# Optimization experiments

Measured on AMD Instinct MI355X. Metric: run time of the kernel, lower is better.

Reference implementation:

```python
import jax, jax.numpy as jnp
import numpy as np

B, N, F, H, N_ITERS = 64, 256, 16, 256, 10


def setup_inputs() -> dict:
    key = jax.random.key(0)
    ks = jax.random.split(key, 20)
    s = 0.05
    jets = jax.random.normal(ks[0], (B, N, F), dtype=jnp.float32)
    # row-normalized dense adjacency (D^-1 A style)
    a = jax.random.uniform(ks[1], (B, N, N), dtype=jnp.float32)
    dads = a / jnp.sum(a, axis=-1, keepdims=True)
    p = lambda k, sh: jax.random.normal(k, sh, dtype=jnp.float32) * s
    return {
        'jets': jets, 'dads': dads,
        'W_emb': p(ks[2], (F, H)), 'b_emb': jnp.zeros((H,), jnp.float32),
        'W_msg': p(ks[3], (H, H)), 'b_msg': jnp.zeros((H,), jnp.float32),
        # GRU vertex update: input = concat(message[H], s[F]) -> H
        'Wz': p(ks[4], (H + F, H)), 'Uz': p(ks[5], (H, H)), 'bz': jnp.zeros((H,), jnp.float32),
        'Wr': p(ks[6], (H + F, H)), 'Ur': p(ks[7], (H, H)), 'br': jnp.zeros((H,), jnp.float32),
        'Wh': p(ks[8], (H + F, H)), 'Uh': p(ks[9], (H, H)), 'bh': jnp.zeros((H,), jnp.float32),
        'W_r1': p(ks[10], (H, H)), 'b_r1': jnp.zeros((H,), jnp.float32),
        'W_r2': p(ks[11], (H, H)), 'b_r2': jnp.zeros((H,), jnp.float32),
    }


def reference(jets, dads, W_emb, b_emb, W_msg, b_msg,
              Wz, Uz, bz, Wr, Ur, br, Wh, Uh, bh,
              W_r1, b_r1, W_r2, b_r2):
    # Embedding: [B,N,F] -> [B,N,H]
    h = jnp.tanh(jets @ W_emb + b_emb)
    for _ in range(N_ITERS):
        # Message: linear then adjacency aggregation + tanh
        m = jnp.tanh(jnp.matmul(dads, h @ W_msg + b_msg))  # [B,N,H]
        # GRU-style vertex update; input = concat(message, original features s)
        x = jnp.concatenate([m, jets], axis=-1)            # [B,N,H+F]
        z = jax.nn.sigmoid(x @ Wz + h @ Uz + bz)
        r = jax.nn.sigmoid(x @ Wr + h @ Ur + br)
        h_tilde = jnp.tanh(x @ Wh + (r * h) @ Uh + bh)
        h = (1.0 - z) * h + z * h_tilde
    # Readout: per-node MLP then sum over nodes -> [B,H]
    out = jnp.sum(jnp.tanh(h @ W_r1 + b_r1) @ W_r2 + b_r2, axis=1)
    return out
```

## Files before the change

### kernel.cpp

```cpp
#include <hip/hip_runtime.h>

#define DEVI __device__ __forceinline__

typedef __attribute__((ext_vector_type(4))) float f32x4;
typedef __attribute__((ext_vector_type(8))) short s16x8;
typedef __attribute__((ext_vector_type(4))) short s16x4;
typedef unsigned short u16;
typedef unsigned int u32;

#define WST 288
#define SROW 264
#define AST 260

#define WAITVM(n) __builtin_amdgcn_s_waitcnt(((n)&0xF) | 0x70 | 0xF00 | (((n)>>4)<<14))

DEVI u16 f2bf(float x){
  u32 u = __float_as_uint(x);
  u = (u + 0x7fffu + ((u >> 16) & 1u)) >> 16;
  return (u16)u;
}
DEVI float bf2f(u16 v){ return __uint_as_float(((u32)v) << 16); }

DEVI float fsigm(float x){ return __builtin_amdgcn_rcpf(1.f + __builtin_amdgcn_exp2f(-1.442695041f * x)); }
DEVI float ftanh(float x){ float e = __builtin_amdgcn_exp2f(2.885390082f * x); return 1.f - 2.f * __builtin_amdgcn_rcpf(e + 1.f); }

DEVI s16x8 ld8(const u16* p){ return *(const s16x8*)p; }
DEVI s16x8 ldb64p(const u16* p){
  s16x4 lo = *(const s16x4*)p;
  s16x4 hi = *(const s16x4*)(p + 4);
  s16x8 r;
  r[0]=lo[0]; r[1]=lo[1]; r[2]=lo[2]; r[3]=lo[3];
  r[4]=hi[0]; r[5]=hi[1]; r[6]=hi[2]; r[7]=hi[3];
  return r;
}

DEVI f32x4 ld4bf(const u16* p){
  uint2 v = *(const uint2*)p;
  f32x4 r;
  r[0] = bf2f((u16)(v.x & 0xffff)); r[1] = bf2f((u16)(v.x >> 16));
  r[2] = bf2f((u16)(v.y & 0xffff)); r[3] = bf2f((u16)(v.y >> 16));
  return r;
}

DEVI void st4bf(u16* p, float a, float b, float c, float d){
  uint2 v;
  v.x = (u32)f2bf(a) | ((u32)f2bf(b) << 16);
  v.y = (u32)f2bf(c) | ((u32)f2bf(d) << 16);
  *(uint2*)p = v;
}

#define MFMA(a,b,c) __builtin_amdgcn_mfma_f32_16x16x32_bf16((a),(b),(c),0,0,0)

DEVI void dma_tile32(const u16* gbase, int rowStride, int c, u16* ldsbase, int lane){
#pragma unroll
  for(int q = 0; q < 2; q++){
    int rw  = lane >> 2;
    int col = ((lane & 3) ^ ((rw >> 1) & 3)) * 8;
    const u16* g = gbase + (size_t)(q*16 + rw)*rowStride + c*32 + col;
    __builtin_amdgcn_global_load_lds((__attribute__((address_space(1))) void*)g,
                                     (__attribute__((address_space(3))) void*)(ldsbase + q*512),
                                     16, 0, 0);
  }
}
#define AFRAG(buf, t) ld8(&(buf)[(t)*512 + ln*32 + ((qd ^ ((ln>>1)&3))*8)])

__global__ void k_prep(
  const float* __restrict__ jets, const float* __restrict__ dads, const float* __restrict__ W_emb,
  const float* __restrict__ W_msg, const float* __restrict__ Wz, const float* __restrict__ Uz,
  const float* __restrict__ Wr, const float* __restrict__ Ur, const float* __restrict__ Wh,
  const float* __restrict__ Uh, const float* __restrict__ W_r1,
  u16* __restrict__ jp, u16* __restrict__ dadsb, u16* __restrict__ Wet, u16* __restrict__ Wmt,
  u16* __restrict__ Wzt, u16* __restrict__ Uzt, u16* __restrict__ Wrt, u16* __restrict__ Urt,
  u16* __restrict__ Wht, u16* __restrict__ Uht, u16* __restrict__ Wr1t)
{
  int blk = blockIdx.x, tid = threadIdx.x;
  if(blk < 1280){
    int mi = blk >> 8, k = blk & 255, j = tid;
    const float* src; u16* dst;
    switch(mi){
      case 0: src = W_msg; dst = Wmt;  break;
      case 1: src = Uz;    dst = Uzt;  break;
      case 2: src = Ur;    dst = Urt;  break;
      case 3: src = Uh;    dst = Uht;  break;
      default: src = W_r1; dst = Wr1t; break;
    }
    dst[j*256 + k] = f2bf(src[k*256 + j]);
  } else if(blk < 2144){
    int q = blk - 1280; int mi = q / 288; int k = q - mi*288; int j = tid;
    const float* src; u16* dst;
    switch(mi){ case 0: src = Wz; dst = Wzt; break; case 1: src = Wr; dst = Wrt; break; default: src = Wh; dst = Wht; break; }
    dst[j*WST + k] = (k < 272) ? f2bf(src[k*256 + j]) : (u16)0;
  } else if(blk < 2176){
    int idx = (blk - 2144)*256 + tid;
    int j = idx >> 5, k = idx & 31;
    Wet[idx] = (k < 16) ? f2bf(W_emb[k*256 + j]) : (u16)0;
  } else if(blk < 4224){
    int idx = (blk - 2176)*256 + tid;
    int n = idx >> 5, k = idx & 31;
    jp[idx] = (k < 16) ? f2bf(jets[n*16 + k]) : (u16)0;
  } else {
    int idx = (blk - 4224)*256 + tid;
    f32x4 v = *(const f32x4*)(dads + (size_t)idx*4);
    st4bf(dadsb + (size_t)idx*4, v[0], v[1], v[2], v[3]);
  }
}

__global__ __launch_bounds__(256,3) void k_embed(
  u16* __restrict__ h, u16* __restrict__ hmo,
  const u16* __restrict__ jp, const u16* __restrict__ Wet, const float* __restrict__ be,
  const u16* __restrict__ Wmt, const float* __restrict__ bm)
{
  __shared__ u16 hbuf[16*SROW];
  const int tid = threadIdx.x;
  const int wv = tid >> 6, lane = tid & 63, ln = lane & 15, qd = lane >> 4;
  const int n0 = blockIdx.x * 16;
  const int b  = n0 >> 8;
  const int nb = n0 & 255;
  const int nodeA = n0 + ln;

  s16x8 jfr = ld8(jp + (size_t)nodeA*32 + qd*8);
#pragma unroll
  for(int t = 0; t < 4; t++){
    int j0 = (wv*4 + t) * 16;
    f32x4 acc = {0.f,0.f,0.f,0.f};
    s16x8 a = ld8(Wet + (size_t)(j0 + ln)*32 + qd*8);
    acc = MFMA(a, jfr, acc);
    f32x4 bv = *(const f32x4*)(be + j0 + qd*4);
    f32x4 hv;
#pragma unroll
    for(int r = 0; r < 4; r++) hv[r] = ftanh(acc[r] + bv[r]);
    st4bf(h + (size_t)nodeA*256 + j0 + qd*4, hv[0], hv[1], hv[2], hv[3]);
    st4bf(&hbuf[ln*SROW + j0 + qd*4], hv[0], hv[1], hv[2], hv[3]);
  }
  __syncthreads();

  s16x8 af[8];
#pragma unroll
  for(int c = 0; c < 8; c++) af[c] = ld8(&hbuf[ln*SROW + c*32 + qd*8]);
#pragma unroll
  for(int tp = 0; tp < 2; tp++){
    int j0 = (wv*4 + tp*2) * 16, j1 = j0 + 16;
    f32x4 a0 = {0.f,0.f,0.f,0.f}, a1 = {0.f,0.f,0.f,0.f};
#pragma unroll
    for(int c = 0; c < 8; c++){
      a0 = MFMA(af[c], ld8(Wmt + (size_t)(j0 + ln)*256 + c*32 + qd*8), a0);
      a1 = MFMA(af[c], ld8(Wmt + (size_t)(j1 + ln)*256 + c*32 + qd*8), a1);
    }
    float b0 = bm[j0 + ln], b1 = bm[j1 + ln];
    st4bf(hmo + (size_t)(b*256 + j0 + ln)*256 + nb + qd*4, a0[0]+b0, a0[1]+b0, a0[2]+b0, a0[3]+b0);
    st4bf(hmo + (size_t)(b*256 + j1 + ln)*256 + nb + qd*4, a1[0]+b1, a1[1]+b1, a1[2]+b1, a1[3]+b1);
  }
}

__global__ __launch_bounds__(512,1) void k_gru(
  u16* __restrict__ h,
  const u16* __restrict__ hmi, u16* __restrict__ hmo,
  const u16* __restrict__ dadsb, const u16* __restrict__ jp,
  const u16* __restrict__ Wzt, const u16* __restrict__ Wrt, const u16* __restrict__ Wht,
  const u16* __restrict__ Uzt, const u16* __restrict__ Urt, const u16* __restrict__ Uht,
  const u16* __restrict__ Wmt,
  const float* __restrict__ bz, const float* __restrict__ br, const float* __restrict__ bhb,
  const float* __restrict__ bm)
{
  __shared__ u16 smM[64*AST];
  __shared__ u16 smB[64*AST];
  __shared__ __align__(16) u16 stg[8][2][2][1024];
  const int tid = threadIdx.x;
  const int wv = tid >> 6, lane = tid & 63, ln = lane & 15, qd = lane >> 4;
  const int blk   = blockIdx.x;
  const int batch = (blk & 7) * 8 + (blk >> 5);
  const int group = (blk >> 3) & 3;
  const int n0 = batch * 256 + group * 64;
  const int b  = batch;
  const int nb = group * 64;
  const int j0w = wv * 32;

  u16* s0 = &stg[wv][0][0][0];
  u16* s1 = &stg[wv][1][0][0];
  u16* u0 = &stg[wv][0][1][0];
  u16* u1 = &stg[wv][1][1][0];

  s16x8 jB[4];
#pragma unroll
  for(int i = 0; i < 4; i++) jB[i] = ld8(jp + (size_t)(n0 + i*16 + ln)*32 + qd*8);

  {
    const u16* gA = hmi + (size_t)(b*256 + j0w)*256;
    f32x4 acc[2][4];
#pragma unroll
    for(int t = 0; t < 2; t++)
#pragma unroll
      for(int i = 0; i < 4; i++) acc[t][i] = (f32x4){0.f,0.f,0.f,0.f};
    dma_tile32(gA, 256, 0, s0, lane);
    s16x8 Bf[4], Bn[4];
#pragma unroll
    for(int i = 0; i < 4; i++) Bf[i] = ld8(dadsb + (size_t)(n0 + i*16 + ln)*256 + qd*8);
#pragma unroll
    for(int c = 0; c < 8; c++){
      u16* cur = (c & 1) ? s1 : s0;
      if(c < 7){
        dma_tile32(gA, 256, c+1, (c & 1) ? s0 : s1, lane);
#pragma unroll
        for(int i = 0; i < 4; i++) Bn[i] = ld8(dadsb + (size_t)(n0 + i*16 + ln)*256 + (c+1)*32 + qd*8);
        WAITVM(6);
      } else {
        WAITVM(0);
      }
#pragma unroll
      for(int t = 0; t < 2; t++){
        s16x8 A = AFRAG(cur, t);
#pragma unroll
        for(int i = 0; i < 4; i++) acc[t][i] = MFMA(A, Bf[i], acc[t][i]);
      }
      if(c < 7){
#pragma unroll
        for(int i = 0; i < 4; i++) Bf[i] = Bn[i];
      }
    }
#pragma unroll
    for(int t = 0; t < 2; t++)
#pragma unroll
      for(int i = 0; i < 4; i++)
        st4bf(&smM[(i*16 + ln)*AST + j0w + t*16 + qd*4],
              ftanh(acc[t][i][0]), ftanh(acc[t][i][1]), ftanh(acc[t][i][2]), ftanh(acc[t][i][3]));
  }
  __syncthreads();

  {
    const u16* gW = Wrt + (size_t)j0w*WST;
    const u16* gU = Urt + (size_t)j0w*256;
    f32x4 acc[2][4];
#pragma unroll
    for(int t = 0; t < 2; t++)
#pragma unroll
      for(int i = 0; i < 4; i++) acc[t][i] = (f32x4){0.f,0.f,0.f,0.f};
    s16x8 Aj[2];
#pragma unroll
    for(int t = 0; t < 2; t++) Aj[t] = ld8(Wrt + (size_t)(j0w + t*16 + ln)*WST + 256 + qd*8);
    dma_tile32(gW, WST, 0, s0, lane);
    dma_tile32(gU, 256, 0, u0, lane);
    s16x8 Bh[4], Bn[4];
#pragma unroll
    for(int i = 0; i < 4; i++) Bh[i] = ld8(h + (size_t)(n0 + i*16 + ln)*256 + qd*8);
#pragma unroll
    for(int c = 0; c < 8; c++){
      u16* cw = (c & 1) ? s1 : s0;
      u16* cu = (c & 1) ? u1 : u0;
      if(c < 7){
        dma_tile32(gW, WST, c+1, (c & 1) ? s0 : s1, lane);
        dma_tile32(gU, 256, c+1, (c & 1) ? u0 : u1, lane);
#pragma unroll
        for(int i = 0; i < 4; i++) Bn[i] = ld8(h + (size_t)(n0 + i*16 + ln)*256 + (c+1)*32 + qd*8);
        WAITVM(8);
      } else {
        WAITVM(0);
      }
      s16x8 Bm[4];
#pragma unroll
      for(int i = 0; i < 4; i++) Bm[i] = ldb64p(&smM[(i*16 + ln)*AST + c*32 + qd*8]);
#pragma unroll
      for(int t = 0; t < 2; t++){
        s16x8 Aw = AFRAG(cw, t);
#pragma unroll
        for(int i = 0; i < 4; i++) acc[t][i] = MFMA(Aw, Bm[i], acc[t][i]);
      }
#pragma unroll
      for(int t = 0; t < 2; t++){
        s16x8 Au = AFRAG(cu, t);
#pragma unroll
        for(int i = 0; i < 4; i++) acc[t][i] = MFMA(Au, Bh[i], acc[t][i]);
      }
      if(c < 7){
#pragma unroll
        for(int i = 0; i < 4; i++) Bh[i] = Bn[i];
      }
    }
#pragma unroll
    for(int t = 0; t < 2; t++)
#pragma unroll
      for(int i = 0; i < 4; i++) acc[t][i] = MFMA(Aj[t], jB[i], acc[t][i]);
#pragma unroll
    for(int t = 0; t < 2; t++){
      f32x4 bv = *(const f32x4*)(br + j0w + t*16 + qd*4);
#pragma unroll
      for(int i = 0; i < 4; i++){
        f32x4 hv = ld4bf(h + (size_t)(n0 + i*16 + ln)*256 + j0w + t*16 + qd*4);
        st4bf(&smB[(i*16 + ln)*AST + j0w + t*16 + qd*4],
              fsigm(acc[t][i][0]+bv[0])*hv[0], fsigm(acc[t][i][1]+bv[1])*hv[1],
              fsigm(acc[t][i][2]+bv[2])*hv[2], fsigm(acc[t][i][3]+bv[3])*hv[3]);
      }
    }
  }
  __syncthreads();

  f32x4 zacc[2][4], gacc[2][4];
#pragma unroll
  for(int t = 0; t < 2; t++)
#pragma unroll
    for(int i = 0; i < 4; i++) zacc[t][i] = (f32x4){0.f,0.f,0.f,0.f};
  {
    const u16* gW = Wzt + (size_t)j0w*WST;
    const u16* gU = Uzt + (size_t)j0w*256;
    s16x8 Aj[2];
#pragma unroll
    for(int t = 0; t < 2; t++) Aj[t] = ld8(Wzt + (size_t)(j0w + t*16 + ln)*WST + 256 + qd*8);
    dma_tile32(gW, WST, 0, s0, lane);
    dma_tile32(gU, 256, 0, u0, lane);
    s16x8 Bh[4], Bn[4];
#pragma unroll
    for(int i = 0; i < 4; i++) Bh[i] = ld8(h + (size_t)(n0 + i*16 + ln)*256 + qd*8);
#pragma unroll
    for(int c = 0; c < 8; c++){
      u16* cw = (c & 1) ? s1 : s0;
      u16* cu = (c & 1) ? u1 : u0;
      if(c < 7){
        dma_tile32(gW, WST, c+1, (c & 1) ? s0 : s1, lane);
        dma_tile32(gU, 256, c+1, (c & 1) ? u0 : u1, lane);
#pragma unroll
        for(int i = 0; i < 4; i++) Bn[i] = ld8(h + (size_t)(n0 + i*16 + ln)*256 + (c+1)*32 + qd*8);
        WAITVM(8);
      } else {
        WAITVM(0);
      }
      s16x8 Bm[4];
#pragma unroll
      for(int i = 0; i < 4; i++) Bm[i] = ldb64p(&smM[(i*16 + ln)*AST + c*32 + qd*8]);
#pragma unroll
      for(int t = 0; t < 2; t++){
        s16x8 Aw = AFRAG(cw, t);
#pragma unroll
        for(int i = 0; i < 4; i++) zacc[t][i] = MFMA(Aw, Bm[i], zacc[t][i]);
      }
#pragma unroll
      for(int t = 0; t < 2; t++){
        s16x8 Au = AFRAG(cu, t);
#pragma unroll
        for(int i = 0; i < 4; i++) zacc[t][i] = MFMA(Au, Bh[i], zacc[t][i]);
      }
      if(c < 7){
#pragma unroll
        for(int i = 0; i < 4; i++) Bh[i] = Bn[i];
      }
    }
#pragma unroll
    for(int t = 0; t < 2; t++)
#pragma unroll
      for(int i = 0; i < 4; i++) zacc[t][i] = MFMA(Aj[t], jB[i], zacc[t][i]);
  }

#pragma unroll
  for(int t = 0; t < 2; t++)
#pragma unroll
    for(int i = 0; i < 4; i++) gacc[t][i] = (f32x4){0.f,0.f,0.f,0.f};
  {
    const u16* gW = Wht + (size_t)j0w*WST;
    const u16* gU = Uht + (size_t)j0w*256;
    s16x8 Aj[2];
#pragma unroll
    for(int t = 0; t < 2; t++) Aj[t] = ld8(Wht + (size_t)(j0w + t*16 + ln)*WST + 256 + qd*8);
    dma_tile32(gW, WST, 0, s0, lane);
    dma_tile32(gU, 256, 0, u0, lane);
#pragma unroll
    for(int c = 0; c < 8; c++){
      u16* cw = (c & 1) ? s1 : s0;
      u16* cu = (c & 1) ? u1 : u0;
      if(c < 7){
        dma_tile32(gW, WST, c+1, (c & 1) ? s0 : s1, lane);
        dma_tile32(gU, 256, c+1, (c & 1) ? u0 : u1, lane);
        WAITVM(4);
      } else {
        WAITVM(0);
      }
      s16x8 Bm[4], Brh[4];
#pragma unroll
      for(int i = 0; i < 4; i++){
        Bm[i]  = ldb64p(&smM[(i*16 + ln)*AST + c*32 + qd*8]);
        Brh[i] = ldb64p(&smB[(i*16 + ln)*AST + c*32 + qd*8]);
      }
#pragma unroll
      for(int t = 0; t < 2; t++){
        s16x8 Aw = AFRAG(cw, t);
#pragma unroll
        for(int i = 0; i < 4; i++) gacc[t][i] = MFMA(Aw, Bm[i], gacc[t][i]);
      }
#pragma unroll
      for(int t = 0; t < 2; t++){
        s16x8 Au = AFRAG(cu, t);
#pragma unroll
        for(int i = 0; i < 4; i++) gacc[t][i] = MFMA(Au, Brh[i], gacc[t][i]);
      }
    }
#pragma unroll
    for(int t = 0; t < 2; t++)
#pragma unroll
      for(int i = 0; i < 4; i++) gacc[t][i] = MFMA(Aj[t], jB[i], gacc[t][i]);
  }
  __syncthreads();

#pragma unroll
  for(int t = 0; t < 2; t++){
    f32x4 bzv = *(const f32x4*)(bz + j0w + t*16 + qd*4);
    f32x4 bhv = *(const f32x4*)(bhb + j0w + t*16 + qd*4);
#pragma unroll
    for(int i = 0; i < 4; i++){
      f32x4 hv = ld4bf(h + (size_t)(n0 + i*16 + ln)*256 + j0w + t*16 + qd*4);
      f32x4 hn;
#pragma unroll
      for(int r = 0; r < 4; r++){
        float z  = fsigm(zacc[t][i][r] + bzv[r]);
        float th = ftanh(gacc[t][i][r] + bhv[r]);
        hn[r] = hv[r] + z * (th - hv[r]);
      }
      st4bf(h + (size_t)(n0 + i*16 + ln)*256 + j0w + t*16 + qd*4, hn[0], hn[1], hn[2], hn[3]);
      st4bf(&smM[(i*16 + ln)*AST + j0w + t*16 + qd*4], hn[0], hn[1], hn[2], hn[3]);
    }
  }
  __syncthreads();

  {
    const u16* gA = Wmt + (size_t)j0w*256;
    f32x4 acc[2][4];
#pragma unroll
    for(int t = 0; t < 2; t++)
#pragma unroll
      for(int i = 0; i < 4; i++) acc[t][i] = (f32x4){0.f,0.f,0.f,0.f};
    dma_tile32(gA, 256, 0, s0, lane);
#pragma unroll
    for(int c = 0; c < 8; c++){
      u16* cur = (c & 1) ? s1 : s0;
      if(c < 7){
        dma_tile32(gA, 256, c+1, (c & 1) ? s0 : s1, lane);
        WAITVM(2);
      } else {
        WAITVM(0);
      }
      s16x8 Bf[4];
#pragma unroll
      for(int i = 0; i < 4; i++) Bf[i] = ldb64p(&smM[(i*16 + ln)*AST + c*32 + qd*8]);
#pragma unroll
      for(int t = 0; t < 2; t++){
        s16x8 A = AFRAG(cur, t);
#pragma unroll
        for(int i = 0; i < 4; i++) acc[t][i] = MFMA(A, Bf[i], acc[t][i]);
      }
    }
#pragma unroll
    for(int t = 0; t < 2; t++){
      f32x4 bmv = *(const f32x4*)(bm + j0w + t*16 + qd*4);
#pragma unroll
      for(int i = 0; i < 4; i++){
#pragma unroll
        for(int r = 0; r < 4; r++){
          hmo[(size_t)(b*256 + j0w + t*16 + qd*4 + r)*256 + nb + i*16 + ln] =
            f2bf(acc[t][i][r] + bmv[r]);
        }
      }
    }
  }
}

__global__ __launch_bounds__(256,3) void k_t(
  const u16* __restrict__ h, u16* __restrict__ t_out,
  const u16* __restrict__ Wr1t, const float* __restrict__ br1)
{
  const int tid = threadIdx.x;
  const int wv = tid >> 6, lane = tid & 63, ln = lane & 15, qd = lane >> 4;
  const int n0 = blockIdx.x * 16;
  const int nodeA = n0 + ln;

  s16x8 hfr[8];
#pragma unroll
  for(int c = 0; c < 8; c++) hfr[c] = ld8(h + (size_t)nodeA*256 + c*32 + qd*8);
#pragma unroll
  for(int tp = 0; tp < 2; tp++){
    int j0 = (wv*4 + tp*2) * 16, j1 = j0 + 16;
    f32x4 a0 = {0.f,0.f,0.f,0.f}, a1 = {0.f,0.f,0.f,0.f};
#pragma unroll
    for(int c = 0; c < 8; c++){
      a0 = MFMA(ld8(Wr1t + (size_t)(j0 + ln)*256 + c*32 + qd*8), hfr[c], a0);
      a1 = MFMA(ld8(Wr1t + (size_t)(j1 + ln)*256 + c*32 + qd*8), hfr[c], a1);
    }
    f32x4 b0 = *(const f32x4*)(br1 + j0 + qd*4);
    f32x4 b1 = *(const f32x4*)(br1 + j1 + qd*4);
    st4bf(t_out + (size_t)nodeA*256 + j0 + qd*4,
          ftanh(a0[0]+b0[0]), ftanh(a0[1]+b0[1]), ftanh(a0[2]+b0[2]), ftanh(a0[3]+b0[3]));
    st4bf(t_out + (size_t)nodeA*256 + j1 + qd*4,
          ftanh(a1[0]+b1[0]), ftanh(a1[1]+b1[1]), ftanh(a1[2]+b1[2]), ftanh(a1[3]+b1[3]));
  }
}

__global__ void k_sum(const u16* __restrict__ t, float* __restrict__ s4){
  int blk = blockIdx.x, tid = threadIdx.x;
  int b = blk >> 2, q = blk & 3;
  float acc = 0.f;
  for(int i = 0; i < 64; i++){
    int n = q*64 + i;
    acc += bf2f(t[(size_t)(b*256 + n)*256 + tid]);
  }
  s4[blk*256 + tid] = acc;
}

__global__ void k_out(const float* __restrict__ s4, const float* __restrict__ W_r2,
                      const float* __restrict__ b_r2, float* __restrict__ out){
  int b = blockIdx.x, j = threadIdx.x;
  float acc = 256.f * b_r2[j];
  for(int k = 0; k < 256; k++){
    float sv = s4[(b*4+0)*256 + k] + s4[(b*4+1)*256 + k] + s4[(b*4+2)*256 + k] + s4[(b*4+3)*256 + k];
    acc += sv * W_r2[k*256 + j];
  }
  out[b*256 + j] = acc;
}

extern "C" void kernel_launch(void* const* d_in, const int* in_sizes, int n_in,
                              void* d_out, int out_size, void* d_ws, size_t ws_size,
                              hipStream_t stream)
{
  const float* jets  = (const float*)d_in[0];
  const float* dads  = (const float*)d_in[1];
  const float* W_emb = (const float*)d_in[2];
  const float* b_emb = (const float*)d_in[3];
  const float* W_msg = (const float*)d_in[4];
  const float* b_msg = (const float*)d_in[5];
  const float* Wz    = (const float*)d_in[6];
  const float* Uz    = (const float*)d_in[7];
  const float* bz    = (const float*)d_in[8];
  const float* Wr    = (const float*)d_in[9];
  const float* Ur    = (const float*)d_in[10];
  const float* br    = (const float*)d_in[11];
  const float* Wh    = (const float*)d_in[12];
  const float* Uh    = (const float*)d_in[13];
  const float* bh    = (const float*)d_in[14];
  const float* W_r1  = (const float*)d_in[15];
  const float* b_r1  = (const float*)d_in[16];
  const float* W_r2  = (const float*)d_in[17];
  const float* b_r2  = (const float*)d_in[18];

  char* ws = (char*)d_ws;
  u16* h      = (u16*)(ws);
  u16* hmA    = (u16*)(ws + 8388608);
  u16* hmB    = (u16*)(ws + 16777216);
  u16* dadsb  = (u16*)(ws + 25165824);
  u16* jp     = (u16*)(ws + 33554432);
  u16* Wmt    = (u16*)(ws + 34603008);
  u16* Uzt    = (u16*)(ws + 34734080);
  u16* Urt    = (u16*)(ws + 34865152);
  u16* Uht    = (u16*)(ws + 34996224);
  u16* Wr1t   = (u16*)(ws + 35127296);
  u16* Wzt    = (u16*)(ws + 35258368);
  u16* Wrt    = (u16*)(ws + 35405824);
  u16* Wht    = (u16*)(ws + 35553280);
  u16* Wet    = (u16*)(ws + 35700736);
  float* s4   = (float*)(ws + 35717120);
  float* outp = (float*)d_out;

  k_prep<<<8320, 256, 0, stream>>>(jets, dads, W_emb, W_msg, Wz, Uz, Wr, Ur, Wh, Uh, W_r1,
                                   jp, dadsb, Wet, Wmt, Wzt, Uzt, Wrt, Urt, Wht, Uht, Wr1t);
  k_embed<<<1024, 256, 0, stream>>>(h, hmA, jp, Wet, b_emb, Wmt, b_msg);
  for(int it = 0; it < 10; ++it){
    const u16* hin = (it & 1) ? hmB : hmA;
    u16* hout      = (it & 1) ? hmA : hmB;
    k_gru<<<256, 512, 0, stream>>>(h, hin, hout, dadsb, jp,
                                   Wzt, Wrt, Wht, Uzt, Urt, Uht, Wmt,
                                   bz, br, bh, b_msg);
  }
  k_t<<<1024, 256, 0, stream>>>(h, hmB, Wr1t, b_r1);
  k_sum<<<256, 256, 0, stream>>>(hmB, s4);
  k_out<<<64, 256, 0, stream>>>(s4, W_r2, b_r2, outp);
}
```

Before: 605.7 us.

## Prefetch next-phase weight tiles before barriers, widen LDS loads, fuse readout kernels

Weight-tile DMA for each GRU phase now starts before the preceding __syncthreads, so the global-to-LDS transfer overlaps the barrier and the epilogue of the previous phase. Per-lane DMA addresses are computed once and reused across chunks. The LDS row stride becomes 264, which allows single 128-bit reads of the smM/smB fragments instead of two 64-bit halves, at some risk of bank conflicts. The k_sum and k_out readout kernels are merged into one launch with 64 blocks, trading parallelism in the node sum for one fewer launch.

```diff
diff --git a/kernel.cpp b/kernel.cpp
--- a/kernel.cpp
+++ b/kernel.cpp
@@ -4,13 +4,12 @@
 
 typedef __attribute__((ext_vector_type(4))) float f32x4;
 typedef __attribute__((ext_vector_type(8))) short s16x8;
-typedef __attribute__((ext_vector_type(4))) short s16x4;
 typedef unsigned short u16;
 typedef unsigned int u32;
 
 #define WST 288
 #define SROW 264
-#define AST 260
+#define AST 264
 
 #define WAITVM(n) __builtin_amdgcn_s_waitcnt(((n)&0xF) | 0x70 | 0xF00 | (((n)>>4)<<14))
 
@@ -25,14 +24,6 @@
 DEVI float ftanh(float x){ float e = __builtin_amdgcn_exp2f(2.885390082f * x); return 1.f - 2.f * __builtin_amdgcn_rcpf(e + 1.f); }
 
 DEVI s16x8 ld8(const u16* p){ return *(const s16x8*)p; }
-DEVI s16x8 ldb64p(const u16* p){
-  s16x4 lo = *(const s16x4*)p;
-  s16x4 hi = *(const s16x4*)(p + 4);
-  s16x8 r;
-  r[0]=lo[0]; r[1]=lo[1]; r[2]=lo[2]; r[3]=lo[3];
-  r[4]=hi[0]; r[5]=hi[1]; r[6]=hi[2]; r[7]=hi[3];
-  return r;
-}
 
 DEVI f32x4 ld4bf(const u16* p){
   uint2 v = *(const uint2*)p;
@@ -51,13 +42,11 @@
 
 #define MFMA(a,b,c) __builtin_amdgcn_mfma_f32_16x16x32_bf16((a),(b),(c),0,0,0)
 
-DEVI void dma_tile32(const u16* gbase, int rowStride, int c, u16* ldsbase, int lane){
+DEVI void dma2(const u16* lanebase, int rowStrideElems, int c, u16* ldsbase){
 #pragma unroll
   for(int q = 0; q < 2; q++){
-    int rw  = lane >> 2;
-    int col = ((lane & 3) ^ ((rw >> 1) & 3)) * 8;
-    const u16* g = gbase + (size_t)(q*16 + rw)*rowStride + c*32 + col;
-    __builtin_amdgcn_global_load_lds((__attribute__((address_space(1))) void*)g,
+    const u16* g = lanebase + (size_t)q*16*rowStrideElems + c*32;
+    __builtin_amdgcn_global_load_lds((__attribute__((address_space(1))) const void*)g,
                                      (__attribute__((address_space(3))) void*)(ldsbase + q*512),
                                      16, 0, 0);
   }
@@ -180,18 +169,22 @@
   u16* u0 = &stg[wv][0][1][0];
   u16* u1 = &stg[wv][1][1][0];
 
+  const int rw = lane >> 2;
+  const int cs = ((lane & 3) ^ ((lane >> 3) & 3)) * 8;
+
+  const u16* laneA = hmi + (size_t)(b*256 + j0w + rw)*256 + cs;
+  dma2(laneA, 256, 0, s0);
+
   s16x8 jB[4];
 #pragma unroll
   for(int i = 0; i < 4; i++) jB[i] = ld8(jp + (size_t)(n0 + i*16 + ln)*32 + qd*8);
 
   {
-    const u16* gA = hmi + (size_t)(b*256 + j0w)*256;
     f32x4 acc[2][4];
 #pragma unroll
     for(int t = 0; t < 2; t++)
 #pragma unroll
       for(int i = 0; i < 4; i++) acc[t][i] = (f32x4){0.f,0.f,0.f,0.f};
-    dma_tile32(gA, 256, 0, s0, lane);
     s16x8 Bf[4], Bn[4];
 #pragma unroll
     for(int i = 0; i < 4; i++) Bf[i] = ld8(dadsb + (size_t)(n0 + i*16 + ln)*256 + qd*8);
@@ -199,7 +192,7 @@
     for(int c = 0; c < 8; c++){
       u16* cur = (c & 1) ? s1 : s0;
       if(c < 7){
-        dma_tile32(gA, 256, c+1, (c & 1) ? s0 : s1, lane);
+        dma2(laneA, 256, c+1, (c & 1) ? s0 : s1);
 #pragma unroll
         for(int i = 0; i < 4; i++) Bn[i] = ld8(dadsb + (size_t)(n0 + i*16 + ln)*256 + (c+1)*32 + qd*8);
         WAITVM(6);
@@ -224,11 +217,13 @@
         st4bf(&smM[(i*16 + ln)*AST + j0w + t*16 + qd*4],
               ftanh(acc[t][i][0]), ftanh(acc[t][i][1]), ftanh(acc[t][i][2]), ftanh(acc[t][i][3]));
   }
+  const u16* laneWr = Wrt + (size_t)(j0w + rw)*WST + cs;
+  const u16* laneUr = Urt + (size_t)(j0w + rw)*256 + cs;
+  dma2(laneWr, WST, 0, s0);
+  dma2(laneUr, 256, 0, u0);
   __syncthreads();
 
   {
-    const u16* gW = Wrt + (size_t)j0w*WST;
-    const u16* gU = Urt + (size_t)j0w*256;
     f32x4 acc[2][4];
 #pragma unroll
     for(int t = 0; t < 2; t++)
@@ -237,8 +232,6 @@
     s16x8 Aj[2];
 #pragma unroll
     for(int t = 0; t < 2; t++) Aj[t] = ld8(Wrt + (size_t)(j0w + t*16 + ln)*WST + 256 + qd*8);
-    dma_tile32(gW, WST, 0, s0, lane);
-    dma_tile32(gU, 256, 0, u0, lane);
     s16x8 Bh[4], Bn[4];
 #pragma unroll
     for(int i = 0; i < 4; i++) Bh[i] = ld8(h + (size_t)(n0 + i*16 + ln)*256 + qd*8);
@@ -247,8 +240,8 @@
       u16* cw = (c & 1) ? s1 : s0;
       u16* cu = (c & 1) ? u1 : u0;
       if(c < 7){
-        dma_tile32(gW, WST, c+1, (c & 1) ? s0 : s1, lane);
-        dma_tile32(gU, 256, c+1, (c & 1) ? u0 : u1, lane);
+        dma2(laneWr, WST, c+1, (c & 1) ? s0 : s1);
+        dma2(laneUr, 256, c+1, (c & 1) ? u0 : u1);
 #pragma unroll
         for(int i = 0; i < 4; i++) Bn[i] = ld8(h + (size_t)(n0 + i*16 + ln)*256 + (c+1)*32 + qd*8);
         WAITVM(8);
@@ -257,7 +250,7 @@
       }
       s16x8 Bm[4];
 #pragma unroll
-      for(int i = 0; i < 4; i++) Bm[i] = ldb64p(&smM[(i*16 + ln)*AST + c*32 + qd*8]);
+      for(int i = 0; i < 4; i++) Bm[i] = ld8(&smM[(i*16 + ln)*AST + c*32 + qd*8]);
 #pragma unroll
       for(int t = 0; t < 2; t++){
         s16x8 Aw = AFRAG(cw, t);
@@ -291,6 +284,10 @@
       }
     }
   }
+  const u16* laneWz = Wzt + (size_t)(j0w + rw)*WST + cs;
+  const u16* laneUz = Uzt + (size_t)(j0w + rw)*256 + cs;
+  dma2(laneWz, WST, 0, s0);
+  dma2(laneUz, 256, 0, u0);
   __syncthreads();
 
   f32x4 zacc[2][4], gacc[2][4];
@@ -299,13 +296,9 @@
 #pragma unroll
     for(int i = 0; i < 4; i++) zacc[t][i] = (f32x4){0.f,0.f,0.f,0.f};
   {
-    const u16* gW = Wzt + (size_t)j0w*WST;
-    const u16* gU = Uzt + (size_t)j0w*256;
     s16x8 Aj[2];
 #pragma unroll
     for(int t = 0; t < 2; t++) Aj[t] = ld8(Wzt + (size_t)(j0w + t*16 + ln)*WST + 256 + qd*8);
-    dma_tile32(gW, WST, 0, s0, lane);
-    dma_tile32(gU, 256, 0, u0, lane);
     s16x8 Bh[4], Bn[4];
 #pragma unroll
     for(int i = 0; i < 4; i++) Bh[i] = ld8(h + (size_t)(n0 + i*16 + ln)*256 + qd*8);
@@ -314,8 +307,8 @@
       u16* cw = (c & 1) ? s1 : s0;
       u16* cu = (c & 1) ? u1 : u0;
       if(c < 7){
-        dma_tile32(gW, WST, c+1, (c & 1) ? s0 : s1, lane);
-        dma_tile32(gU, 256, c+1, (c & 1) ? u0 : u1, lane);
+        dma2(laneWz, WST, c+1, (c & 1) ? s0 : s1);
+        dma2(laneUz, 256, c+1, (c & 1) ? u0 : u1);
 #pragma unroll
         for(int i = 0; i < 4; i++) Bn[i] = ld8(h + (size_t)(n0 + i*16 + ln)*256 + (c+1)*32 + qd*8);
         WAITVM(8);
@@ -324,7 +317,7 @@
       }
       s16x8 Bm[4];
 #pragma unroll
-      for(int i = 0; i < 4; i++) Bm[i] = ldb64p(&smM[(i*16 + ln)*AST + c*32 + qd*8]);
+      for(int i = 0; i < 4; i++) Bm[i] = ld8(&smM[(i*16 + ln)*AST + c*32 + qd*8]);
 #pragma unroll
       for(int t = 0; t < 2; t++){
         s16x8 Aw = AFRAG(cw, t);
@@ -347,26 +340,27 @@
 #pragma unroll
       for(int i = 0; i < 4; i++) zacc[t][i] = MFMA(Aj[t], jB[i], zacc[t][i]);
   }
+
+  const u16* laneWh = Wht + (size_t)(j0w + rw)*WST + cs;
+  const u16* laneUh = Uht + (size_t)(j0w + rw)*256 + cs;
+  dma2(laneWh, WST, 0, s0);
+  dma2(laneUh, 256, 0, u0);
 
 #pragma unroll
   for(int t = 0; t < 2; t++)
 #pragma unroll
     for(int i = 0; i < 4; i++) gacc[t][i] = (f32x4){0.f,0.f,0.f,0.f};
   {
-    const u16* gW = Wht + (size_t)j0w*WST;
-    const u16* gU = Uht + (size_t)j0w*256;
     s16x8 Aj[2];
 #pragma unroll
     for(int t = 0; t < 2; t++) Aj[t] = ld8(Wht + (size_t)(j0w + t*16 + ln)*WST + 256 + qd*8);
-    dma_tile32(gW, WST, 0, s0, lane);
-    dma_tile32(gU, 256, 0, u0, lane);
 #pragma unroll
     for(int c = 0; c < 8; c++){
       u16* cw = (c & 1) ? s1 : s0;
       u16* cu = (c & 1) ? u1 : u0;
       if(c < 7){
-        dma_tile32(gW, WST, c+1, (c & 1) ? s0 : s1, lane);
-        dma_tile32(gU, 256, c+1, (c & 1) ? u0 : u1, lane);
+        dma2(laneWh, WST, c+1, (c & 1) ? s0 : s1);
+        dma2(laneUh, 256, c+1, (c & 1) ? u0 : u1);
         WAITVM(4);
       } else {
         WAITVM(0);
@@ -374,8 +368,8 @@
       s16x8 Bm[4], Brh[4];
 #pragma unroll
       for(int i = 0; i < 4; i++){
-        Bm[i]  = ldb64p(&smM[(i*16 + ln)*AST + c*32 + qd*8]);
-        Brh[i] = ldb64p(&smB[(i*16 + ln)*AST + c*32 + qd*8]);
+        Bm[i]  = ld8(&smM[(i*16 + ln)*AST + c*32 + qd*8]);
+        Brh[i] = ld8(&smB[(i*16 + ln)*AST + c*32 + qd*8]);
       }
 #pragma unroll
       for(int t = 0; t < 2; t++){
@@ -395,6 +389,8 @@
 #pragma unroll
       for(int i = 0; i < 4; i++) gacc[t][i] = MFMA(Aj[t], jB[i], gacc[t][i]);
   }
+  const u16* laneWm = Wmt + (size_t)(j0w + rw)*256 + cs;
+  dma2(laneWm, 256, 0, s0);
   __syncthreads();
 
 #pragma unroll
@@ -418,25 +414,23 @@
   __syncthreads();
 
   {
-    const u16* gA = Wmt + (size_t)j0w*256;
     f32x4 acc[2][4];
 #pragma unroll
     for(int t = 0; t < 2; t++)
 #pragma unroll
       for(int i = 0; i < 4; i++) acc[t][i] = (f32x4){0.f,0.f,0.f,0.f};
-    dma_tile32(gA, 256, 0, s0, lane);
 #pragma unroll
     for(int c = 0; c < 8; c++){
       u16* cur = (c & 1) ? s1 : s0;
       if(c < 7){
-        dma_tile32(gA, 256, c+1, (c & 1) ? s0 : s1, lane);
+        dma2(laneWm, 256, c+1, (c & 1) ? s0 : s1);
         WAITVM(2);
       } else {
         WAITVM(0);
       }
       s16x8 Bf[4];
 #pragma unroll
-      for(int i = 0; i < 4; i++) Bf[i] = ldb64p(&smM[(i*16 + ln)*AST + c*32 + qd*8]);
+      for(int i = 0; i < 4; i++) Bf[i] = ld8(&smM[(i*16 + ln)*AST + c*32 + qd*8]);
 #pragma unroll
       for(int t = 0; t < 2; t++){
         s16x8 A = AFRAG(cur, t);
@@ -489,26 +483,18 @@
   }
 }
 
-__global__ void k_sum(const u16* __restrict__ t, float* __restrict__ s4){
-  int blk = blockIdx.x, tid = threadIdx.x;
-  int b = blk >> 2, q = blk & 3;
+__global__ void k_red(const u16* __restrict__ t, const float* __restrict__ W_r2,
+                      const float* __restrict__ b_r2, float* __restrict__ out){
+  __shared__ float s[256];
+  int b = blockIdx.x, k = threadIdx.x;
   float acc = 0.f;
-  for(int i = 0; i < 64; i++){
-    int n = q*64 + i;
-    acc += bf2f(t[(size_t)(b*256 + n)*256 + tid]);
-  }
-  s4[blk*256 + tid] = acc;
-}
-
-__global__ void k_out(const float* __restrict__ s4, const float* __restrict__ W_r2,
-                      const float* __restrict__ b_r2, float* __restrict__ out){
-  int b = blockIdx.x, j = threadIdx.x;
-  float acc = 256.f * b_r2[j];
-  for(int k = 0; k < 256; k++){
-    float sv = s4[(b*4+0)*256 + k] + s4[(b*4+1)*256 + k] + s4[(b*4+2)*256 + k] + s4[(b*4+3)*256 + k];
-    acc += sv * W_r2[k*256 + j];
-  }
-  out[b*256 + j] = acc;
+  for(int n = 0; n < 256; n++) acc += bf2f(t[(size_t)(b*256 + n)*256 + k]);
+  s[k] = acc;
+  __syncthreads();
+  int j = threadIdx.x;
+  float o = 256.f * b_r2[j];
+  for(int k2 = 0; k2 < 256; k2++) o += s[k2] * W_r2[k2*256 + j];
+  out[b*256 + j] = o;
 }
 
 extern "C" void kernel_launch(void* const* d_in, const int* in_sizes, int n_in,
@@ -550,7 +536,6 @@
   u16* Wrt    = (u16*)(ws + 35405824);
   u16* Wht    = (u16*)(ws + 35553280);
   u16* Wet    = (u16*)(ws + 35700736);
-  float* s4   = (float*)(ws + 35717120);
   float* outp = (float*)d_out;
 
   k_prep<<<8320, 256, 0, stream>>>(jets, dads, W_emb, W_msg, Wz, Uz, Wr, Ur, Wh, Uh, W_r1,
@@ -564,6 +549,5 @@
                                    bz, br, bh, b_msg);
   }
   k_t<<<1024, 256, 0, stream>>>(h, hmB, Wr1t, b_r1);
-  k_sum<<<256, 256, 0, stream>>>(hmB, s4);
-  k_out<<<64, 256, 0, stream>>>(s4, W_r2, b_r2, outp);
-}
+  k_red<<<64, 256, 0, stream>>>(hmB, W_r2, b_r2, outp);
+}
```

Result: no change. 598.5 us (-1.2%).
